# Kernel optimization log

Measured on AMD Instinct MI355X. Metric: run time of the kernel, lower is better.

The kernel has to match this reference:

```python
import jax, jax.numpy as jnp
import numpy as np

IN_F = 4096
OUT_F = 4096
SPARSITY = 0.9
NNZ = round((1.0 - SPARSITY) * IN_F * OUT_F)  # 1677722
BATCH = 4096


def setup_inputs() -> dict:
    key = jax.random.key(0)
    k1, k2, k3, k4 = jax.random.split(key, 4)
    x = jax.random.normal(k1, (BATCH, IN_F), dtype=jnp.float32)
    # Kaiming-ish scale for sparse fan-in
    weights = jax.random.normal(k2, (NNZ,), dtype=jnp.float32) * 0.02
    row = jax.random.randint(k3, (NNZ,), 0, OUT_F, dtype=jnp.int32)
    col = jax.random.randint(k4, (NNZ,), 0, IN_F, dtype=jnp.int32)
    indices = jnp.stack([row, col], axis=0)  # (2, nnz) like the torch buffer
    active_mask = jnp.ones((NNZ,), dtype=bool)
    return {
        "x": x,
        "weights": weights,
        "indices": indices,
        "active_mask": active_mask,
        "out_features": OUT_F,
        "in_features": IN_F,
    }


def reference(x, weights, indices, active_mask, out_features, in_features):
    # Torch forward: select active edges, build COO (out,in), coalesce
    # (sums duplicate indices), then y = (W @ x^T)^T.
    # Equivalent math: zero inactive weights, scatter-add into dense W,
    # then a dense matmul. Duplicates are summed by .add, matching coalesce.
    w = jnp.where(active_mask, weights, jnp.zeros((), dtype=weights.dtype))
    W = jnp.zeros((out_features, in_features), dtype=x.dtype)
    W = W.at[indices[0], indices[1]].add(w)  # (out, in)
    return x @ W.T  # (B, out)
```

## Files before the change

### kernel.cpp

```cpp
#include <hip/hip_runtime.h>
#include <cstdint>
#include <cstddef>

#define IN_F  4096
#define OUT_F 4096
#define BATCH 4096

typedef __bf16 bf16_t;
typedef __bf16 bf16x8 __attribute__((ext_vector_type(8)));
typedef float  f32x4  __attribute__((ext_vector_type(4)));

__device__ __forceinline__ unsigned short f32_to_bf16_rne(float f) {
  union { float f; unsigned int u; } v;
  v.f = f;
  unsigned int u = v.u;
  return (unsigned short)((u + 0x7FFFu + ((u >> 16) & 1u)) >> 16);
}

__device__ __forceinline__ uint4 cvt8(float4 a, float4 b) {
  uint4 o;
  o.x = (unsigned)f32_to_bf16_rne(a.x) | ((unsigned)f32_to_bf16_rne(a.y) << 16);
  o.y = (unsigned)f32_to_bf16_rne(a.z) | ((unsigned)f32_to_bf16_rne(a.w) << 16);
  o.z = (unsigned)f32_to_bf16_rne(b.x) | ((unsigned)f32_to_bf16_rne(b.y) << 16);
  o.w = (unsigned)f32_to_bf16_rne(b.z) | ((unsigned)f32_to_bf16_rne(b.w) << 16);
  return o;
}

#define XUNITS ((BATCH * IN_F) / 8)

__global__ __launch_bounds__(256) void scatter_cvtx(
    const float* __restrict__ w, const int* __restrict__ rows,
    const int* __restrict__ cols, const int* __restrict__ mask,
    unsigned* __restrict__ Wpk, int nnz,
    const float4* __restrict__ xin, uint4* __restrict__ xbf) {
  const int total = XUNITS + nnz;
  for (int u = blockIdx.x * 256 + threadIdx.x; u < total;
       u += gridDim.x * 256) {
    if (u < XUNITS) {
      xbf[u] = cvt8(xin[2 * u], xin[2 * u + 1]);
    } else {
      const int i = u - XUNITS;
      if (mask[i] != 0) {
        const unsigned h = f32_to_bf16_rne(w[i]);
        const size_t e = (size_t)rows[i] * IN_F + cols[i];
        const unsigned data = (e & 1) ? (h << 16) : h;
        unsigned* p = Wpk + (e >> 1);
        asm volatile("global_atomic_pk_add_bf16 %0, %1, off"
                     :: "v"(p), "v"(data) : "memory");
      }
    }
  }
}

#define A0_B 0
#define B0_B 32768
#define A1_B 65536
#define B1_B 98304
#define HALF 16384

#define STAGE(Xg, kpos, ldsbase) do {                                          \
  __builtin_amdgcn_global_load_lds(                                            \
    (const __attribute__((address_space(1))) void*)((Xg) + (size_t)srow * 4096 + (kpos) + schunk), \
    (__attribute__((address_space(3))) void*)(lds + (ldsbase) + tid * 16), 16, 0, 0); \
  __builtin_amdgcn_global_load_lds(                                            \
    (const __attribute__((address_space(1))) void*)((Xg) + (size_t)(srow + 128) * 4096 + (kpos) + schunk), \
    (__attribute__((address_space(3))) void*)(lds + (ldsbase) + 8192 + tid * 16), 16, 0, 0); \
} while (0)

#define LDA4(base, mh) do {                                                    \
  a0 = *(const bf16x8*)(lds + (base) + offA[mh][0]);                           \
  a1 = *(const bf16x8*)(lds + (base) + offA[mh][1]);                           \
  a2 = *(const bf16x8*)(lds + (base) + offA[mh][2]);                           \
  a3 = *(const bf16x8*)(lds + (base) + offA[mh][3]);                           \
} while (0)

#define LDB4(base) do {                                                        \
  b0 = *(const bf16x8*)(lds + (base) + offB[0]);                               \
  b1 = *(const bf16x8*)(lds + (base) + offB[1]);                               \
  b2 = *(const bf16x8*)(lds + (base) + offB[2]);                               \
  b3 = *(const bf16x8*)(lds + (base) + offB[3]);                               \
} while (0)

#define MFMA16(mh) do {                                                        \
  acc[(mh)*4+0][0] = __builtin_amdgcn_mfma_f32_16x16x32_bf16(a0, b0, acc[(mh)*4+0][0], 0, 0, 0); \
  acc[(mh)*4+0][1] = __builtin_amdgcn_mfma_f32_16x16x32_bf16(a0, b1, acc[(mh)*4+0][1], 0, 0, 0); \
  acc[(mh)*4+0][2] = __builtin_amdgcn_mfma_f32_16x16x32_bf16(a0, b2, acc[(mh)*4+0][2], 0, 0, 0); \
  acc[(mh)*4+0][3] = __builtin_amdgcn_mfma_f32_16x16x32_bf16(a0, b3, acc[(mh)*4+0][3], 0, 0, 0); \
  acc[(mh)*4+1][0] = __builtin_amdgcn_mfma_f32_16x16x32_bf16(a1, b0, acc[(mh)*4+1][0], 0, 0, 0); \
  acc[(mh)*4+1][1] = __builtin_amdgcn_mfma_f32_16x16x32_bf16(a1, b1, acc[(mh)*4+1][1], 0, 0, 0); \
  acc[(mh)*4+1][2] = __builtin_amdgcn_mfma_f32_16x16x32_bf16(a1, b2, acc[(mh)*4+1][2], 0, 0, 0); \
  acc[(mh)*4+1][3] = __builtin_amdgcn_mfma_f32_16x16x32_bf16(a1, b3, acc[(mh)*4+1][3], 0, 0, 0); \
  acc[(mh)*4+2][0] = __builtin_amdgcn_mfma_f32_16x16x32_bf16(a2, b0, acc[(mh)*4+2][0], 0, 0, 0); \
  acc[(mh)*4+2][1] = __builtin_amdgcn_mfma_f32_16x16x32_bf16(a2, b1, acc[(mh)*4+2][1], 0, 0, 0); \
  acc[(mh)*4+2][2] = __builtin_amdgcn_mfma_f32_16x16x32_bf16(a2, b2, acc[(mh)*4+2][2], 0, 0, 0); \
  acc[(mh)*4+2][3] = __builtin_amdgcn_mfma_f32_16x16x32_bf16(a2, b3, acc[(mh)*4+2][3], 0, 0, 0); \
  acc[(mh)*4+3][0] = __builtin_amdgcn_mfma_f32_16x16x32_bf16(a3, b0, acc[(mh)*4+3][0], 0, 0, 0); \
  acc[(mh)*4+3][1] = __builtin_amdgcn_mfma_f32_16x16x32_bf16(a3, b1, acc[(mh)*4+3][1], 0, 0, 0); \
  acc[(mh)*4+3][2] = __builtin_amdgcn_mfma_f32_16x16x32_bf16(a3, b2, acc[(mh)*4+3][2], 0, 0, 0); \
  acc[(mh)*4+3][3] = __builtin_amdgcn_mfma_f32_16x16x32_bf16(a3, b3, acc[(mh)*4+3][3], 0, 0, 0); \
} while (0)

#define BAR()   __builtin_amdgcn_s_barrier()
#define LGKM0() do { asm volatile("s_waitcnt lgkmcnt(0)" ::: "memory");        \
                     __builtin_amdgcn_sched_barrier(0); } while (0)
#define VM(n)   asm volatile("s_waitcnt vmcnt(" #n ")" ::: "memory")
#define PRIO1() __builtin_amdgcn_s_setprio(1)
#define PRIO0() __builtin_amdgcn_s_setprio(0)

__global__ __launch_bounds__(512, 2) void gemm_bt_8ph(
    const bf16_t* __restrict__ A, const bf16_t* __restrict__ Bm,
    float* __restrict__ C) {
  __shared__ __align__(16) char lds[131072];

  const int tid  = threadIdx.x;
  const int lane = tid & 63;
  const int wave = tid >> 6;
  const int wm   = wave >> 2;
  const int wn   = wave & 3;

  const int sbid = (blockIdx.x & 7) * 32 + (blockIdx.x >> 3);
  const int bm   = sbid >> 4;
  const int bn   = sbid & 15;

  const int frow = lane & 15;
  const int c16  = (lane >> 4) * 16;

  int offA[2][4], offB[4];
#pragma unroll
  for (int mh = 0; mh < 2; ++mh)
#pragma unroll
    for (int mi = 0; mi < 4; ++mi) {
      int r = wm * 128 + mh * 64 + mi * 16 + frow;
      offA[mh][mi] = r * 64 + (c16 ^ (((r >> 1) & 3) << 4));
    }
#pragma unroll
  for (int ni = 0; ni < 4; ++ni) {
    int r = wn * 64 + ni * 16 + frow;
    offB[ni] = r * 64 + (c16 ^ (((r >> 1) & 3) << 4));
  }

  const int srow   = tid >> 2;
  const int schunk = ((tid & 3) ^ ((srow >> 1) & 3)) * 8;
  const bf16_t* Ag = A  + (size_t)bm * 256 * 4096;
  const bf16_t* Bg = Bm + (size_t)bn * 256 * 4096;

  f32x4 acc[8][4] = {};
  bf16x8 a0, a1, a2, a3, b0, b1, b2, b3;

  STAGE(Ag, 0,  A0_B);
  STAGE(Bg, 0,  B0_B);
  STAGE(Ag, 32, A0_B + HALF);
  STAGE(Bg, 32, B0_B + HALF);
  STAGE(Ag, 64, A1_B);
  STAGE(Bg, 64, B1_B);
  VM(4);
  BAR();

  int kb = 0;
#pragma unroll 1
  for (int i = 0; i < 31; ++i, kb += 128) {
    LDA4(A0_B, 0); LDB4(B0_B);
    STAGE(Ag, kb + 96, A1_B + HALF);
    BAR(); LGKM0(); PRIO1(); MFMA16(0); PRIO0(); BAR();
    LDA4(A0_B, 1);
    STAGE(Bg, kb + 96, B1_B + HALF);
    BAR(); LGKM0(); PRIO1(); MFMA16(1); PRIO0(); BAR();
    LDA4(A0_B + HALF, 0); LDB4(B0_B + HALF);
    STAGE(Ag, kb + 128, A0_B);
    BAR(); LGKM0(); PRIO1(); MFMA16(0); PRIO0(); BAR();
    LDA4(A0_B + HALF, 1);
    STAGE(Bg, kb + 128, B0_B);
    BAR(); LGKM0(); PRIO1(); MFMA16(1); PRIO0(); VM(4); BAR();
    LDA4(A1_B, 0); LDB4(B1_B);
    STAGE(Ag, kb + 160, A0_B + HALF);
    BAR(); LGKM0(); PRIO1(); MFMA16(0); PRIO0(); BAR();
    LDA4(A1_B, 1);
    STAGE(Bg, kb + 160, B0_B + HALF);
    BAR(); LGKM0(); PRIO1(); MFMA16(1); PRIO0(); BAR();
    LDA4(A1_B + HALF, 0); LDB4(B1_B + HALF);
    STAGE(Ag, kb + 192, A1_B);
    BAR(); LGKM0(); PRIO1(); MFMA16(0); PRIO0(); BAR();
    LDA4(A1_B + HALF, 1);
    STAGE(Bg, kb + 192, B1_B);
    BAR(); LGKM0(); PRIO1(); MFMA16(1); PRIO0(); VM(4); BAR();
  }

  LDA4(A0_B, 0); LDB4(B0_B);
  STAGE(Ag, kb + 96, A1_B + HALF);
  BAR(); LGKM0(); PRIO1(); MFMA16(0); PRIO0(); BAR();
  LDA4(A0_B, 1);
  STAGE(Bg, kb + 96, B1_B + HALF);
  BAR(); LGKM0(); PRIO1(); MFMA16(1); PRIO0(); BAR();
  LDA4(A0_B + HALF, 0); LDB4(B0_B + HALF);
  BAR(); LGKM0(); PRIO1(); MFMA16(0); PRIO0(); BAR();
  LDA4(A0_B + HALF, 1);
  BAR(); LGKM0(); PRIO1(); MFMA16(1); PRIO0(); VM(0); BAR();
  LDA4(A1_B, 0); LDB4(B1_B);
  BAR(); LGKM0(); PRIO1(); MFMA16(0); PRIO0(); BAR();
  LDA4(A1_B, 1);
  BAR(); LGKM0(); PRIO1(); MFMA16(1); PRIO0(); BAR();
  LDA4(A1_B + HALF, 0); LDB4(B1_B + HALF);
  BAR(); LGKM0(); PRIO1(); MFMA16(0); PRIO0(); BAR();
  LDA4(A1_B + HALF, 1);
  LGKM0(); PRIO1(); MFMA16(1); PRIO0();

#pragma unroll
  for (int mh = 0; mh < 2; ++mh)
#pragma unroll
    for (int mi = 0; mi < 4; ++mi)
#pragma unroll
      for (int ni = 0; ni < 4; ++ni) {
        const int row = bm * 256 + wm * 128 + mh * 64 + mi * 16 + (lane >> 4) * 4;
        const int col = bn * 256 + wn * 64 + ni * 16 + frow;
#pragma unroll
        for (int jj = 0; jj < 4; ++jj)
          C[(size_t)(row + jj) * 4096 + col] = acc[mh * 4 + mi][ni][jj];
      }
}

extern "C" void kernel_launch(void* const* d_in, const int* in_sizes, int n_in,
                              void* d_out, int out_size, void* d_ws, size_t ws_size,
                              hipStream_t stream) {
  const float* x     = (const float*)d_in[0];
  const float* wvals = (const float*)d_in[1];
  const int*   idx   = (const int*)d_in[2];
  const int*   mk    = (const int*)d_in[3];
  const int    nnz   = in_sizes[1];

  bf16_t* Wbf = (bf16_t*)d_ws;
  bf16_t* xbf = (bf16_t*)((char*)d_ws + (size_t)OUT_F * IN_F * sizeof(bf16_t));

  const size_t needed = (size_t)OUT_F * IN_F * 2 + (size_t)BATCH * IN_F * 2;
  if (ws_size < needed) return;

  hipMemsetAsync(Wbf, 0, (size_t)OUT_F * IN_F * sizeof(bf16_t), stream);

  scatter_cvtx<<<2048, 256, 0, stream>>>(
      wvals, idx, idx + nnz, mk, (unsigned*)Wbf, nnz,
      (const float4*)x, (uint4*)xbf);

  gemm_bt_8ph<<<256, 512, 0, stream>>>(xbf, Wbf, (float*)d_out);
}
```

Before: 208.3 us.

## Restructure GEMM phases to load B once per K-tile and split M into quarters

Each phase now reads B fragments for both K halves (64 deep) once per 64-wide K-tile and iterates over four 32-row M quarters, doing 16 MFMAs per phase with 2x2 A fragments. The global staging order is reshuffled so B tiles arrive one step ahead of A tiles. The goal is fewer redundant LDS reads of B and a longer MFMA chain per barrier-bounded phase. In exchange it keeps 8 B fragment registers live across phases, which raises register pressure, and it changes the prefetch timing.

```diff
diff --git a/kernel.cpp b/kernel.cpp
--- a/kernel.cpp
+++ b/kernel.cpp
@@ -67,37 +67,31 @@
     (__attribute__((address_space(3))) void*)(lds + (ldsbase) + 8192 + tid * 16), 16, 0, 0); \
 } while (0)
 
-#define LDA4(base, mh) do {                                                    \
-  a0 = *(const bf16x8*)(lds + (base) + offA[mh][0]);                           \
-  a1 = *(const bf16x8*)(lds + (base) + offA[mh][1]);                           \
-  a2 = *(const bf16x8*)(lds + (base) + offA[mh][2]);                           \
-  a3 = *(const bf16x8*)(lds + (base) + offA[mh][3]);                           \
-} while (0)
-
-#define LDB4(base) do {                                                        \
-  b0 = *(const bf16x8*)(lds + (base) + offB[0]);                               \
-  b1 = *(const bf16x8*)(lds + (base) + offB[1]);                               \
-  b2 = *(const bf16x8*)(lds + (base) + offB[2]);                               \
-  b3 = *(const bf16x8*)(lds + (base) + offB[3]);                               \
-} while (0)
-
-#define MFMA16(mh) do {                                                        \
-  acc[(mh)*4+0][0] = __builtin_amdgcn_mfma_f32_16x16x32_bf16(a0, b0, acc[(mh)*4+0][0], 0, 0, 0); \
-  acc[(mh)*4+0][1] = __builtin_amdgcn_mfma_f32_16x16x32_bf16(a0, b1, acc[(mh)*4+0][1], 0, 0, 0); \
-  acc[(mh)*4+0][2] = __builtin_amdgcn_mfma_f32_16x16x32_bf16(a0, b2, acc[(mh)*4+0][2], 0, 0, 0); \
-  acc[(mh)*4+0][3] = __builtin_amdgcn_mfma_f32_16x16x32_bf16(a0, b3, acc[(mh)*4+0][3], 0, 0, 0); \
-  acc[(mh)*4+1][0] = __builtin_amdgcn_mfma_f32_16x16x32_bf16(a1, b0, acc[(mh)*4+1][0], 0, 0, 0); \
-  acc[(mh)*4+1][1] = __builtin_amdgcn_mfma_f32_16x16x32_bf16(a1, b1, acc[(mh)*4+1][1], 0, 0, 0); \
-  acc[(mh)*4+1][2] = __builtin_amdgcn_mfma_f32_16x16x32_bf16(a1, b2, acc[(mh)*4+1][2], 0, 0, 0); \
-  acc[(mh)*4+1][3] = __builtin_amdgcn_mfma_f32_16x16x32_bf16(a1, b3, acc[(mh)*4+1][3], 0, 0, 0); \
-  acc[(mh)*4+2][0] = __builtin_amdgcn_mfma_f32_16x16x32_bf16(a2, b0, acc[(mh)*4+2][0], 0, 0, 0); \
-  acc[(mh)*4+2][1] = __builtin_amdgcn_mfma_f32_16x16x32_bf16(a2, b1, acc[(mh)*4+2][1], 0, 0, 0); \
-  acc[(mh)*4+2][2] = __builtin_amdgcn_mfma_f32_16x16x32_bf16(a2, b2, acc[(mh)*4+2][2], 0, 0, 0); \
-  acc[(mh)*4+2][3] = __builtin_amdgcn_mfma_f32_16x16x32_bf16(a2, b3, acc[(mh)*4+2][3], 0, 0, 0); \
-  acc[(mh)*4+3][0] = __builtin_amdgcn_mfma_f32_16x16x32_bf16(a3, b0, acc[(mh)*4+3][0], 0, 0, 0); \
-  acc[(mh)*4+3][1] = __builtin_amdgcn_mfma_f32_16x16x32_bf16(a3, b1, acc[(mh)*4+3][1], 0, 0, 0); \
-  acc[(mh)*4+3][2] = __builtin_amdgcn_mfma_f32_16x16x32_bf16(a3, b2, acc[(mh)*4+3][2], 0, 0, 0); \
-  acc[(mh)*4+3][3] = __builtin_amdgcn_mfma_f32_16x16x32_bf16(a3, b3, acc[(mh)*4+3][3], 0, 0, 0); \
+#define RDB(base) do {                                                         \
+  _Pragma("unroll")                                                            \
+  for (int ni = 0; ni < 4; ++ni)                                               \
+    _Pragma("unroll")                                                          \
+    for (int kk = 0; kk < 2; ++kk)                                             \
+      b[ni][kk] = *(const bf16x8*)(lds + (base) + kk * HALF + offB[ni]);       \
+} while (0)
+
+#define RDA(base, q) do {                                                      \
+  _Pragma("unroll")                                                            \
+  for (int mi = 0; mi < 2; ++mi)                                               \
+    _Pragma("unroll")                                                          \
+    for (int kk = 0; kk < 2; ++kk)                                             \
+      a[mi][kk] = *(const bf16x8*)(lds + (base) + kk * HALF + offA[q][mi]);    \
+} while (0)
+
+#define MFMAQ(q) do {                                                          \
+  _Pragma("unroll")                                                            \
+  for (int mi = 0; mi < 2; ++mi)                                               \
+    _Pragma("unroll")                                                          \
+    for (int ni = 0; ni < 4; ++ni)                                             \
+      _Pragma("unroll")                                                        \
+      for (int kk = 0; kk < 2; ++kk)                                           \
+        acc[2 * (q) + mi][ni] = __builtin_amdgcn_mfma_f32_16x16x32_bf16(       \
+            a[mi][kk], b[ni][kk], acc[2 * (q) + mi][ni], 0, 0, 0);             \
 } while (0)
 
 #define BAR()   __builtin_amdgcn_s_barrier()
@@ -107,7 +101,7 @@
 #define PRIO1() __builtin_amdgcn_s_setprio(1)
 #define PRIO0() __builtin_amdgcn_s_setprio(0)
 
-__global__ __launch_bounds__(512, 2) void gemm_bt_8ph(
+__global__ __launch_bounds__(512, 2) void gemm_q(
     const bf16_t* __restrict__ A, const bf16_t* __restrict__ Bm,
     float* __restrict__ C) {
   __shared__ __align__(16) char lds[131072];
@@ -125,13 +119,13 @@
   const int frow = lane & 15;
   const int c16  = (lane >> 4) * 16;
 
-  int offA[2][4], offB[4];
-#pragma unroll
-  for (int mh = 0; mh < 2; ++mh)
-#pragma unroll
-    for (int mi = 0; mi < 4; ++mi) {
-      int r = wm * 128 + mh * 64 + mi * 16 + frow;
-      offA[mh][mi] = r * 64 + (c16 ^ (((r >> 1) & 3) << 4));
+  int offA[4][2], offB[4];
+#pragma unroll
+  for (int q = 0; q < 4; ++q)
+#pragma unroll
+    for (int mi = 0; mi < 2; ++mi) {
+      int r = wm * 128 + q * 32 + mi * 16 + frow;
+      offA[q][mi] = r * 64 + (c16 ^ (((r >> 1) & 3) << 4));
     }
 #pragma unroll
   for (int ni = 0; ni < 4; ++ni) {
@@ -145,77 +139,75 @@
   const bf16_t* Bg = Bm + (size_t)bn * 256 * 4096;
 
   f32x4 acc[8][4] = {};
-  bf16x8 a0, a1, a2, a3, b0, b1, b2, b3;
+  bf16x8 a[2][2], b[4][2];
 
   STAGE(Ag, 0,  A0_B);
+  STAGE(Ag, 32, A0_B + HALF);
   STAGE(Bg, 0,  B0_B);
-  STAGE(Ag, 32, A0_B + HALF);
   STAGE(Bg, 32, B0_B + HALF);
-  STAGE(Ag, 64, A1_B);
   STAGE(Bg, 64, B1_B);
+  STAGE(Bg, 96, B1_B + HALF);
   VM(4);
   BAR();
 
   int kb = 0;
 #pragma unroll 1
   for (int i = 0; i < 31; ++i, kb += 128) {
-    LDA4(A0_B, 0); LDB4(B0_B);
+    RDB(B0_B); RDA(A0_B, 0);
+    STAGE(Ag, kb + 64, A1_B);
+    BAR(); LGKM0(); PRIO1(); MFMAQ(0); PRIO0(); BAR();
+    RDA(A0_B, 1);
     STAGE(Ag, kb + 96, A1_B + HALF);
-    BAR(); LGKM0(); PRIO1(); MFMA16(0); PRIO0(); BAR();
-    LDA4(A0_B, 1);
-    STAGE(Bg, kb + 96, B1_B + HALF);
-    BAR(); LGKM0(); PRIO1(); MFMA16(1); PRIO0(); BAR();
-    LDA4(A0_B + HALF, 0); LDB4(B0_B + HALF);
+    BAR(); LGKM0(); PRIO1(); MFMAQ(1); PRIO0(); BAR();
+    RDA(A0_B, 2);
+    STAGE(Bg, kb + 128, B0_B);
+    BAR(); LGKM0(); PRIO1(); MFMAQ(2); PRIO0(); BAR();
+    RDA(A0_B, 3);
+    STAGE(Bg, kb + 160, B0_B + HALF);
+    BAR(); LGKM0(); PRIO1(); MFMAQ(3); PRIO0(); VM(4); BAR();
+    RDB(B1_B); RDA(A1_B, 0);
     STAGE(Ag, kb + 128, A0_B);
-    BAR(); LGKM0(); PRIO1(); MFMA16(0); PRIO0(); BAR();
-    LDA4(A0_B + HALF, 1);
-    STAGE(Bg, kb + 128, B0_B);
-    BAR(); LGKM0(); PRIO1(); MFMA16(1); PRIO0(); VM(4); BAR();
-    LDA4(A1_B, 0); LDB4(B1_B);
+    BAR(); LGKM0(); PRIO1(); MFMAQ(0); PRIO0(); BAR();
+    RDA(A1_B, 1);
     STAGE(Ag, kb + 160, A0_B + HALF);
-    BAR(); LGKM0(); PRIO1(); MFMA16(0); PRIO0(); BAR();
-    LDA4(A1_B, 1);
-    STAGE(Bg, kb + 160, B0_B + HALF);
-    BAR(); LGKM0(); PRIO1(); MFMA16(1); PRIO0(); BAR();
-    LDA4(A1_B + HALF, 0); LDB4(B1_B + HALF);
-    STAGE(Ag, kb + 192, A1_B);
-    BAR(); LGKM0(); PRIO1(); MFMA16(0); PRIO0(); BAR();
-    LDA4(A1_B + HALF, 1);
+    BAR(); LGKM0(); PRIO1(); MFMAQ(1); PRIO0(); BAR();
+    RDA(A1_B, 2);
     STAGE(Bg, kb + 192, B1_B);
-    BAR(); LGKM0(); PRIO1(); MFMA16(1); PRIO0(); VM(4); BAR();
+    BAR(); LGKM0(); PRIO1(); MFMAQ(2); PRIO0(); BAR();
+    RDA(A1_B, 3);
+    STAGE(Bg, kb + 224, B1_B + HALF);
+    BAR(); LGKM0(); PRIO1(); MFMAQ(3); PRIO0(); VM(4); BAR();
   }
 
-  LDA4(A0_B, 0); LDB4(B0_B);
-  STAGE(Ag, kb + 96, A1_B + HALF);
-  BAR(); LGKM0(); PRIO1(); MFMA16(0); PRIO0(); BAR();
-  LDA4(A0_B, 1);
-  STAGE(Bg, kb + 96, B1_B + HALF);
-  BAR(); LGKM0(); PRIO1(); MFMA16(1); PRIO0(); BAR();
-  LDA4(A0_B + HALF, 0); LDB4(B0_B + HALF);
-  BAR(); LGKM0(); PRIO1(); MFMA16(0); PRIO0(); BAR();
-  LDA4(A0_B + HALF, 1);
-  BAR(); LGKM0(); PRIO1(); MFMA16(1); PRIO0(); VM(0); BAR();
-  LDA4(A1_B, 0); LDB4(B1_B);
-  BAR(); LGKM0(); PRIO1(); MFMA16(0); PRIO0(); BAR();
-  LDA4(A1_B, 1);
-  BAR(); LGKM0(); PRIO1(); MFMA16(1); PRIO0(); BAR();
-  LDA4(A1_B + HALF, 0); LDB4(B1_B + HALF);
-  BAR(); LGKM0(); PRIO1(); MFMA16(0); PRIO0(); BAR();
-  LDA4(A1_B + HALF, 1);
-  LGKM0(); PRIO1(); MFMA16(1); PRIO0();
-
-#pragma unroll
-  for (int mh = 0; mh < 2; ++mh)
-#pragma unroll
-    for (int mi = 0; mi < 4; ++mi)
-#pragma unroll
-      for (int ni = 0; ni < 4; ++ni) {
-        const int row = bm * 256 + wm * 128 + mh * 64 + mi * 16 + (lane >> 4) * 4;
-        const int col = bn * 256 + wn * 64 + ni * 16 + frow;
-#pragma unroll
-        for (int jj = 0; jj < 4; ++jj)
-          C[(size_t)(row + jj) * 4096 + col] = acc[mh * 4 + mi][ni][jj];
-      }
+  RDB(B0_B); RDA(A0_B, 0);
+  STAGE(Ag, 4032, A1_B);
+  BAR(); LGKM0(); PRIO1(); MFMAQ(0); PRIO0(); BAR();
+  RDA(A0_B, 1);
+  STAGE(Ag, 4064, A1_B + HALF);
+  BAR(); LGKM0(); PRIO1(); MFMAQ(1); PRIO0(); BAR();
+  RDA(A0_B, 2);
+  BAR(); LGKM0(); PRIO1(); MFMAQ(2); PRIO0(); BAR();
+  RDA(A0_B, 3);
+  BAR(); LGKM0(); PRIO1(); MFMAQ(3); PRIO0(); VM(0); BAR();
+  RDB(B1_B); RDA(A1_B, 0);
+  BAR(); LGKM0(); PRIO1(); MFMAQ(0); PRIO0(); BAR();
+  RDA(A1_B, 1);
+  BAR(); LGKM0(); PRIO1(); MFMAQ(1); PRIO0(); BAR();
+  RDA(A1_B, 2);
+  BAR(); LGKM0(); PRIO1(); MFMAQ(2); PRIO0(); BAR();
+  RDA(A1_B, 3);
+  LGKM0(); PRIO1(); MFMAQ(3); PRIO0();
+
+#pragma unroll
+  for (int m = 0; m < 8; ++m)
+#pragma unroll
+    for (int ni = 0; ni < 4; ++ni) {
+      const int row = bm * 256 + wm * 128 + m * 16 + (lane >> 4) * 4;
+      const int col = bn * 256 + wn * 64 + ni * 16 + frow;
+#pragma unroll
+      for (int jj = 0; jj < 4; ++jj)
+        C[(size_t)(row + jj) * 4096 + col] = acc[m][ni][jj];
+    }
 }
 
 extern "C" void kernel_launch(void* const* d_in, const int* in_sizes, int n_in,
@@ -239,5 +231,5 @@
       wvals, idx, idx + nnz, mk, (unsigned*)Wbf, nnz,
       (const float4*)x, (uint4*)xbf);
 
-  gemm_bt_8ph<<<256, 512, 0, stream>>>(xbf, Wbf, (float*)d_out);
-}
+  gemm_q<<<256, 512, 0, stream>>>(xbf, Wbf, (float*)d_out);
+}
```

Measured after the change: 203.6 us. 2.3% less time.
